# Kernel optimization log

Hardware: AMD Instinct MI355X
Metric: run time of the kernel (lower is better)

## Reference

```python
import jax, jax.numpy as jnp
import numpy as np

N_NODES = 50000
N_EDGES = 800000
IN_DIM = 128
HID_DIM = 128
EMB_DIM = 64


def _glorot(key, shape):
    fan_in, fan_out = shape
    lim = np.sqrt(6.0 / (fan_in + fan_out))
    return jax.random.uniform(key, shape, jnp.float32, -lim, lim)


def setup_inputs() -> dict:
    key = jax.random.key(0)
    ks = jax.random.split(key, 5)
    x = jax.random.normal(ks[0], (N_NODES, IN_DIM), jnp.float32)
    edge_index = jax.random.randint(ks[1], (2, N_EDGES), 0, N_NODES, jnp.int64)
    W1 = _glorot(ks[2], (IN_DIM, HID_DIM))
    W2 = _glorot(ks[3], (HID_DIM, EMB_DIM))
    W3 = _glorot(ks[4], (EMB_DIM, IN_DIM))
    b1 = jnp.zeros((HID_DIM,), jnp.float32)
    b2 = jnp.zeros((EMB_DIM,), jnp.float32)
    b3 = jnp.zeros((IN_DIM,), jnp.float32)
    return {"x": x, "edge_index": edge_index,
            "W1": W1, "b1": b1, "W2": W2, "b2": b2, "W3": W3, "b3": b3}


def _gcn_conv(x, W, b, src, dst, norm, n_nodes):
    # PyG GCNConv: transform then normalized neighbor aggregation (with self-loops)
    h = x @ W                                   # [N, out]
    msg = h[src] * norm[:, None]                # gather + scale, [E+N, out]
    out = jax.ops.segment_sum(msg, dst, num_segments=n_nodes)  # scatter-add
    return out + b


def _gcn_norm(edge_index, n_nodes):
    # add self-loops, compute sym-normalized edge weights D^-1/2 (A+I) D^-1/2
    loop = jnp.arange(n_nodes, dtype=edge_index.dtype)
    src = jnp.concatenate([edge_index[0], loop])
    dst = jnp.concatenate([edge_index[1], loop])
    deg = jax.ops.segment_sum(jnp.ones_like(dst, jnp.float32), dst,
                              num_segments=n_nodes)
    dinv = jnp.where(deg > 0, jax.lax.rsqrt(jnp.maximum(deg, 1.0)), 0.0)
    norm = dinv[src] * dinv[dst]
    return src, dst, norm


def reference(x, edge_index, W1, b1, W2, b2, W3, b3):
    n_nodes = x.shape[0]
    src, dst, norm = _gcn_norm(edge_index, n_nodes)
    h = jax.nn.relu(_gcn_conv(x, W1, b1, src, dst, norm, n_nodes))
    h = jax.nn.relu(_gcn_conv(h, W2, b2, src, dst, norm, n_nodes))
    out = _gcn_conv(h, W3, b3, src, dst, norm, n_nodes)
    return out
```

## Files before the change

kernel.cpp:

```cpp
#include <hip/hip_runtime.h>
#include <hip/hip_bf16.h>

static inline int ceil_div(int a, int b) { return (a + b - 1) / b; }


__global__ void count_kernel(const int* __restrict__ ei, int* __restrict__ deg,
        int* __restrict__ rank, int E) {
    int e = blockIdx.x * blockDim.x + threadIdx.x;
    if (e < E) rank[e] = atomicAdd(&deg[ei[E + e]], 1);
}


__global__ __launch_bounds__(256) void block_sum_kernel(const int* __restrict__ deg,
        int* __restrict__ bsum, int n) {
    int base = blockIdx.x * 1024 + (int)threadIdx.x * 4;
    int s = 0;
    #pragma unroll
    for (int j = 0; j < 4; ++j) { int i = base + j; if (i < n) s += deg[i]; }
    #pragma unroll
    for (int off = 32; off > 0; off >>= 1) s += __shfl_down(s, off);
    __shared__ int ws[4];
    int wid = (int)threadIdx.x >> 6, lane = (int)threadIdx.x & 63;
    if (lane == 0) ws[wid] = s;
    __syncthreads();
    if (threadIdx.x == 0) bsum[blockIdx.x] = ws[0] + ws[1] + ws[2] + ws[3];
}

__global__ void scan_bsum_kernel(const int* __restrict__ bsum, int* __restrict__ boff,
        int* __restrict__ rowptr, int nb, int n) {
    int tid = (int)threadIdx.x;
    int v = (tid < nb) ? bsum[tid] : 0;
    #pragma unroll
    for (int off = 1; off < 64; off <<= 1) {
        int u = __shfl_up(v, off);
        if (tid >= off) v += u;
    }
    if (tid < nb) boff[tid + 1] = v;
    if (tid == 0) boff[0] = 0;
    if (tid == nb - 1) rowptr[n] = v;
}

__global__ __launch_bounds__(256) void scan_apply_kernel(const int* __restrict__ deg,
        const int* __restrict__ boff, int* __restrict__ rowptr,
        float* __restrict__ dinv, int n) {
    int tid = (int)threadIdx.x;
    int base = blockIdx.x * 1024 + tid * 4;
    int d[4];
    #pragma unroll
    for (int j = 0; j < 4; ++j) { int i = base + j; d[j] = (i < n) ? deg[i] : 0; }
    int tsum = d[0] + d[1] + d[2] + d[3];
    int v = tsum;
    int lane = tid & 63, wid = tid >> 6;
    #pragma unroll
    for (int off = 1; off < 64; off <<= 1) {
        int u = __shfl_up(v, off);
        if (lane >= off) v += u;
    }
    __shared__ int wsum[4];
    if (lane == 63) wsum[wid] = v;
    __syncthreads();
    int wbase = 0;
    #pragma unroll
    for (int w = 0; w < 4; ++w) if (w < wid) wbase += wsum[w];
    int run = boff[blockIdx.x] + wbase + (v - tsum);
    #pragma unroll
    for (int j = 0; j < 4; ++j) {
        int i = base + j;
        if (i < n) {
            rowptr[i] = run;
            dinv[i] = rsqrtf((float)(d[j] + 1));
        }
        run += d[j];
    }
}

__global__ void fill_kernel(const int* __restrict__ ei, const int* __restrict__ rowptr,
        const int* __restrict__ rank, int* __restrict__ colidx, int E) {
    int e = blockIdx.x * blockDim.x + threadIdx.x;
    if (e < E) {
        int s = ei[e];
        int d = ei[E + e];
        colidx[rowptr[d] + rank[e]] = s;
    }
}


template<int K, int N, bool BIAS, bool OUT_BF16>
__global__ __launch_bounds__(256) void gemm_kernel(const float* __restrict__ A,
        const float* __restrict__ W, const float* __restrict__ bias,
        void* __restrict__ out_, int M) {
    __shared__ float As[16][68];
    __shared__ float Bs[16][68];
    const int bm = blockIdx.x * 64;
    const int bn = blockIdx.y * 64;
    const int tid = (int)threadIdx.x;
    const int tx = tid & 15;
    const int ty = tid >> 4;
    float acc[4][4] = {};
    for (int k0 = 0; k0 < K; k0 += 16) {
        {
            int m   = tid >> 2;
            int kk4 = (tid & 3) * 4;
            float4 v = make_float4(0.f, 0.f, 0.f, 0.f);
            if (bm + m < M)
                v = *(const float4*)&A[(size_t)(bm + m) * K + k0 + kk4];
            As[kk4 + 0][m] = v.x;
            As[kk4 + 1][m] = v.y;
            As[kk4 + 2][m] = v.z;
            As[kk4 + 3][m] = v.w;
        }
        {
            int kk = tid >> 4;
            int n4 = (tid & 15) * 4;
            *(float4*)&Bs[kk][n4] = *(const float4*)&W[(size_t)(k0 + kk) * N + bn + n4];
        }
        __syncthreads();
        #pragma unroll
        for (int kk = 0; kk < 16; ++kk) {
            float4 a4 = *(const float4*)&As[kk][ty * 4];
            float4 b4 = *(const float4*)&Bs[kk][tx * 4];
            float a[4] = {a4.x, a4.y, a4.z, a4.w};
            float b[4] = {b4.x, b4.y, b4.z, b4.w};
            #pragma unroll
            for (int i = 0; i < 4; ++i)
                #pragma unroll
                for (int j = 0; j < 4; ++j)
                    acc[i][j] += a[i] * b[j];
        }
        __syncthreads();
    }
    #pragma unroll
    for (int i = 0; i < 4; ++i) {
        int m = bm + ty * 4 + i;
        if (m >= M) continue;
        float v[4];
        #pragma unroll
        for (int j = 0; j < 4; ++j) {
            v[j] = acc[i][j];
            if (BIAS) v[j] += bias[bn + tx * 4 + j];
        }
        size_t base = (size_t)m * N + bn + tx * 4;
        if constexpr (OUT_BF16) {
            __hip_bfloat16* ob = (__hip_bfloat16*)out_;
            __hip_bfloat162 p0, p1;
            p0.x = __float2bfloat16(v[0]); p0.y = __float2bfloat16(v[1]);
            p1.x = __float2bfloat16(v[2]); p1.y = __float2bfloat16(v[3]);
            *(__hip_bfloat162*)&ob[base]     = p0;
            *(__hip_bfloat162*)&ob[base + 2] = p1;
        } else {
            float* of = (float*)out_;
            *(float2*)&of[base]     = make_float2(v[0], v[1]);
            *(float2*)&of[base + 2] = make_float2(v[2], v[3]);
        }
    }
}


template<int D, bool BIAS, bool RELU, bool OUT_BF16>
__global__ __launch_bounds__(256) void agg_kernel(const void* __restrict__ in_,
        const float* __restrict__ bias,
        const int* __restrict__ rowptr, const int* __restrict__ colidx,
        const float* __restrict__ dinv, void* __restrict__ out_, int n) {
    constexpr int VPL = D / 64;
    const int lane = (int)threadIdx.x & 63;
    const int wid  = (int)threadIdx.x >> 6;
    const int i = blockIdx.x * 4 + wid;
    if (i >= n) return;
    const float di = dinv[i];
    float acc0 = 0.f, acc1 = 0.f;
    if constexpr (VPL == 2) {
        const __hip_bfloat162* in = (const __hip_bfloat162*)in_;
        __hip_bfloat162 sv = in[(size_t)i * 64 + lane];
        acc0 = di * __bfloat162float(sv.x);
        acc1 = di * __bfloat162float(sv.y);
    } else {
        const __hip_bfloat16* in = (const __hip_bfloat16*)in_;
        acc0 = di * __bfloat162float(in[(size_t)i * 64 + lane]);
    }
    int e = rowptr[i];
    const int e1 = rowptr[i + 1];
    for (; e + 8 <= e1; e += 8) {
        int s[8]; float w[8];
        #pragma unroll
        for (int j = 0; j < 8; ++j) s[j] = __builtin_amdgcn_readfirstlane(colidx[e + j]);
        #pragma unroll
        for (int j = 0; j < 8; ++j) w[j] = dinv[s[j]];
        if constexpr (VPL == 2) {
            const __hip_bfloat162* in = (const __hip_bfloat162*)in_;
            __hip_bfloat162 v[8];
            #pragma unroll
            for (int j = 0; j < 8; ++j) v[j] = in[(size_t)s[j] * 64 + lane];
            #pragma unroll
            for (int j = 0; j < 8; ++j) {
                acc0 += w[j] * __bfloat162float(v[j].x);
                acc1 += w[j] * __bfloat162float(v[j].y);
            }
        } else {
            const __hip_bfloat16* in = (const __hip_bfloat16*)in_;
            __hip_bfloat16 v[8];
            #pragma unroll
            for (int j = 0; j < 8; ++j) v[j] = in[(size_t)s[j] * 64 + lane];
            #pragma unroll
            for (int j = 0; j < 8; ++j) acc0 += w[j] * __bfloat162float(v[j]);
        }
    }
    for (; e < e1; ++e) {
        int s = __builtin_amdgcn_readfirstlane(colidx[e]);
        float w = dinv[s];
        if constexpr (VPL == 2) {
            const __hip_bfloat162* in = (const __hip_bfloat162*)in_;
            __hip_bfloat162 v = in[(size_t)s * 64 + lane];
            acc0 += w * __bfloat162float(v.x);
            acc1 += w * __bfloat162float(v.y);
        } else {
            const __hip_bfloat16* in = (const __hip_bfloat16*)in_;
            acc0 += w * __bfloat162float(in[(size_t)s * 64 + lane]);
        }
    }
    float v0 = di * acc0;
    float v1 = di * acc1;
    if constexpr (VPL == 2) {
        if (BIAS) { v0 += bias[2 * lane]; v1 += bias[2 * lane + 1]; }
        if (RELU) { v0 = fmaxf(v0, 0.f); v1 = fmaxf(v1, 0.f); }
        if constexpr (OUT_BF16) {
            __hip_bfloat162* ob = (__hip_bfloat162*)out_;
            __hip_bfloat162 p; p.x = __float2bfloat16(v0); p.y = __float2bfloat16(v1);
            ob[(size_t)i * 64 + lane] = p;
        } else {
            float2* of = (float2*)out_;
            of[(size_t)i * 64 + lane] = make_float2(v0, v1);
        }
    } else {
        if (BIAS) v0 += bias[lane];
        if (RELU) v0 = fmaxf(v0, 0.f);
        if constexpr (OUT_BF16) {
            __hip_bfloat16* ob = (__hip_bfloat16*)out_;
            ob[(size_t)i * 64 + lane] = __float2bfloat16(v0);
        } else {
            float* of = (float*)out_;
            of[(size_t)i * 64 + lane] = v0;
        }
    }
}


extern "C" void kernel_launch(void* const* d_in, const int* in_sizes, int n_in,
                              void* d_out, int out_size, void* d_ws, size_t ws_size,
                              hipStream_t stream) {
    const float* x  = (const float*)d_in[0];
    const int*   ei = (const int*)d_in[1];
    const float* W1 = (const float*)d_in[2];
    const float* b1 = (const float*)d_in[3];
    const float* W2 = (const float*)d_in[4];
    const float* b2 = (const float*)d_in[5];
    const float* W3 = (const float*)d_in[6];
    const float* b3 = (const float*)d_in[7];

    const int IN = 128;
    const int n  = in_sizes[0] / IN;
    const int E  = in_sizes[1] / 2;

    char* ws = (char*)d_ws;
    size_t off = 0;
    auto alloc = [&](size_t bytes) {
        char* p = ws + off;
        off += (bytes + 255) & ~(size_t)255;
        return p;
    };
    __hip_bfloat16* hA_bf = (__hip_bfloat16*)alloc((size_t)n * 128 * 2);
    float*          bufB  = (float*)alloc((size_t)n * 128 * 4);
    __hip_bfloat16* hC_bf = (__hip_bfloat16*)alloc((size_t)n * 64 * 2);
    __hip_bfloat16* hD_bf = (__hip_bfloat16*)alloc((size_t)n * 64 * 2);
    float*          bufE  = (float*)alloc((size_t)n * 64 * 4);
    int*   deg    = (int*)  alloc((size_t)n * sizeof(int));
    int*   rowptr = (int*)  alloc(((size_t)n + 1) * sizeof(int));
    float* dinv   = (float*)alloc((size_t)n * sizeof(float));
    int*   colidx = (int*)  alloc((size_t)E * sizeof(int));
    int*   rank   = (int*)  alloc((size_t)E * sizeof(int));
    int*   bsum   = (int*)  alloc(64 * sizeof(int));
    int*   boff   = (int*)  alloc(65 * sizeof(int));

    const int nb = ceil_div(n, 1024);

    hipMemsetAsync(deg, 0, (size_t)n * sizeof(int), stream);
    count_kernel<<<ceil_div(E, 256), 256, 0, stream>>>(ei, deg, rank, E);
    block_sum_kernel<<<nb, 256, 0, stream>>>(deg, bsum, n);
    scan_bsum_kernel<<<1, 64, 0, stream>>>(bsum, boff, rowptr, nb, n);
    scan_apply_kernel<<<nb, 256, 0, stream>>>(deg, boff, rowptr, dinv, n);
    fill_kernel<<<ceil_div(E, 256), 256, 0, stream>>>(ei, rowptr, rank, colidx, E);

    dim3 g1(ceil_div(n, 64), 2);
    gemm_kernel<128, 128, false, true><<<g1, 256, 0, stream>>>(x, W1, nullptr, hA_bf, n);
    agg_kernel<128, true, true, false><<<ceil_div(n, 4), 256, 0, stream>>>(
        hA_bf, b1, rowptr, colidx, dinv, bufB, n);

    dim3 g2(ceil_div(n, 64), 1);
    gemm_kernel<128, 64, false, true><<<g2, 256, 0, stream>>>(bufB, W2, nullptr, hC_bf, n);
    agg_kernel<64, true, true, true><<<ceil_div(n, 4), 256, 0, stream>>>(
        hC_bf, b2, rowptr, colidx, dinv, hD_bf, n);

    agg_kernel<64, false, false, false><<<ceil_div(n, 4), 256, 0, stream>>>(
        hD_bf, nullptr, rowptr, colidx, dinv, bufE, n);
    dim3 g3(ceil_div(n, 64), 2);
    gemm_kernel<64, 128, true, false><<<g3, 256, 0, stream>>>(bufE, W3, b3, d_out, n);
}
```

Before: 305.8 us.

## Build CSR with two-level bucketed counting sort using shared-memory atomics

```diff
diff --git a/kernel.cpp b/kernel.cpp
--- a/kernel.cpp
+++ b/kernel.cpp
@@ -4,83 +4,102 @@
 static inline int ceil_div(int a, int b) { return (a + b - 1) / b; }
 
 
-__global__ void count_kernel(const int* __restrict__ ei, int* __restrict__ deg,
-        int* __restrict__ rank, int E) {
-    int e = blockIdx.x * blockDim.x + threadIdx.x;
-    if (e < E) rank[e] = atomicAdd(&deg[ei[E + e]], 1);
-}
-
-
-__global__ __launch_bounds__(256) void block_sum_kernel(const int* __restrict__ deg,
-        int* __restrict__ bsum, int n) {
-    int base = blockIdx.x * 1024 + (int)threadIdx.x * 4;
-    int s = 0;
-    #pragma unroll
-    for (int j = 0; j < 4; ++j) { int i = base + j; if (i < n) s += deg[i]; }
-    #pragma unroll
-    for (int off = 32; off > 0; off >>= 1) s += __shfl_down(s, off);
-    __shared__ int ws[4];
-    int wid = (int)threadIdx.x >> 6, lane = (int)threadIdx.x & 63;
-    if (lane == 0) ws[wid] = s;
-    __syncthreads();
-    if (threadIdx.x == 0) bsum[blockIdx.x] = ws[0] + ws[1] + ws[2] + ws[3];
-}
-
-__global__ void scan_bsum_kernel(const int* __restrict__ bsum, int* __restrict__ boff,
-        int* __restrict__ rowptr, int nb, int n) {
-    int tid = (int)threadIdx.x;
-    int v = (tid < nb) ? bsum[tid] : 0;
-    #pragma unroll
-    for (int off = 1; off < 64; off <<= 1) {
-        int u = __shfl_up(v, off);
-        if (tid >= off) v += u;
-    }
-    if (tid < nb) boff[tid + 1] = v;
-    if (tid == 0) boff[0] = 0;
-    if (tid == nb - 1) rowptr[n] = v;
-}
-
-__global__ __launch_bounds__(256) void scan_apply_kernel(const int* __restrict__ deg,
-        const int* __restrict__ boff, int* __restrict__ rowptr,
-        float* __restrict__ dinv, int n) {
-    int tid = (int)threadIdx.x;
-    int base = blockIdx.x * 1024 + tid * 4;
-    int d[4];
-    #pragma unroll
-    for (int j = 0; j < 4; ++j) { int i = base + j; d[j] = (i < n) ? deg[i] : 0; }
-    int tsum = d[0] + d[1] + d[2] + d[3];
-    int v = tsum;
-    int lane = tid & 63, wid = tid >> 6;
-    #pragma unroll
-    for (int off = 1; off < 64; off <<= 1) {
-        int u = __shfl_up(v, off);
-        if (lane >= off) v += u;
-    }
-    __shared__ int wsum[4];
-    if (lane == 63) wsum[wid] = v;
-    __syncthreads();
-    int wbase = 0;
-    #pragma unroll
-    for (int w = 0; w < 4; ++w) if (w < wid) wbase += wsum[w];
-    int run = boff[blockIdx.x] + wbase + (v - tsum);
-    #pragma unroll
-    for (int j = 0; j < 4; ++j) {
-        int i = base + j;
-        if (i < n) {
-            rowptr[i] = run;
-            dinv[i] = rsqrtf((float)(d[j] + 1));
-        }
-        run += d[j];
-    }
-}
-
-__global__ void fill_kernel(const int* __restrict__ ei, const int* __restrict__ rowptr,
-        const int* __restrict__ rank, int* __restrict__ colidx, int E) {
-    int e = blockIdx.x * blockDim.x + threadIdx.x;
-    if (e < E) {
+#define CSR_NBLK 64
+
+__global__ __launch_bounds__(1024) void bucket_hist_kernel(const int* __restrict__ ei,
+        int* __restrict__ hist_b, int E, int nbucket, int chunk) {
+    __shared__ int h[512];
+    for (int i = threadIdx.x; i < nbucket; i += blockDim.x) h[i] = 0;
+    __syncthreads();
+    const int b = blockIdx.x;
+    const int e0 = b * chunk, e1 = min(E, e0 + chunk);
+    for (int e = e0 + (int)threadIdx.x; e < e1; e += blockDim.x)
+        atomicAdd(&h[ei[E + e] >> 8], 1);
+    __syncthreads();
+    for (int i = threadIdx.x; i < nbucket; i += blockDim.x)
+        hist_b[i * CSR_NBLK + b] = h[i];
+}
+
+__global__ __launch_bounds__(512) void bucket_scan_kernel(int* __restrict__ hist_b,
+        int* __restrict__ bucket_start, int nbucket, int E) {
+    __shared__ int sc[512];
+    const int t = (int)threadIdx.x;
+    int tot = 0;
+    if (t < nbucket) {
+        #pragma unroll 8
+        for (int b = 0; b < CSR_NBLK; ++b) tot += hist_b[t * CSR_NBLK + b];
+    }
+    sc[t] = tot;
+    __syncthreads();
+    for (int off = 1; off < 512; off <<= 1) {
+        int v = (t >= off) ? sc[t - off] : 0;
+        __syncthreads();
+        sc[t] += v;
+        __syncthreads();
+    }
+    if (t < nbucket) {
+        int excl = sc[t] - tot;
+        bucket_start[t] = excl;
+        int base = excl;
+        #pragma unroll 8
+        for (int b = 0; b < CSR_NBLK; ++b) {
+            int c = hist_b[t * CSR_NBLK + b];
+            hist_b[t * CSR_NBLK + b] = base;
+            base += c;
+        }
+    }
+    if (t == 0) bucket_start[nbucket] = E;
+}
+
+__global__ __launch_bounds__(1024) void bucket_scatter_kernel(const int* __restrict__ ei,
+        const int* __restrict__ base_b, int2* __restrict__ tmp, int E, int nbucket, int chunk) {
+    __shared__ int cur[512];
+    const int b = blockIdx.x;
+    for (int i = threadIdx.x; i < nbucket; i += blockDim.x)
+        cur[i] = base_b[i * CSR_NBLK + b];
+    __syncthreads();
+    const int e0 = b * chunk, e1 = min(E, e0 + chunk);
+    for (int e = e0 + (int)threadIdx.x; e < e1; e += blockDim.x) {
         int s = ei[e];
         int d = ei[E + e];
-        colidx[rowptr[d] + rank[e]] = s;
+        int pos = atomicAdd(&cur[d >> 8], 1);
+        tmp[pos] = make_int2(s, d);
+    }
+}
+
+__global__ __launch_bounds__(256) void csr_build_kernel(const int2* __restrict__ tmp,
+        const int* __restrict__ bucket_start, int* __restrict__ rowptr,
+        float* __restrict__ dinv, int* __restrict__ colidx, int n, int E) {
+    __shared__ int hist[256], sc[256], cur[256];
+    const int h = blockIdx.x;
+    const int t = (int)threadIdx.x;
+    hist[t] = 0;
+    __syncthreads();
+    const int e0 = bucket_start[h], e1 = bucket_start[h + 1];
+    for (int e = e0 + t; e < e1; e += 256)
+        atomicAdd(&hist[tmp[e].y & 255], 1);
+    __syncthreads();
+    sc[t] = hist[t];
+    __syncthreads();
+    for (int off = 1; off < 256; off <<= 1) {
+        int v = (t >= off) ? sc[t - off] : 0;
+        __syncthreads();
+        sc[t] += v;
+        __syncthreads();
+    }
+    const int excl = sc[t] - hist[t];
+    const int node = h * 256 + t;
+    if (node < n) {
+        rowptr[node] = e0 + excl;
+        dinv[node] = rsqrtf((float)(hist[t] + 1));
+    }
+    if (h == 0 && t == 0) rowptr[n] = E;
+    cur[t] = excl;
+    __syncthreads();
+    for (int e = e0 + t; e < e1; e += 256) {
+        int2 p = tmp[e];
+        int pos = e0 + atomicAdd(&cur[p.y & 255], 1);
+        colidx[pos] = p.x;
     }
 }
 
@@ -272,22 +291,20 @@
     __hip_bfloat16* hC_bf = (__hip_bfloat16*)alloc((size_t)n * 64 * 2);
     __hip_bfloat16* hD_bf = (__hip_bfloat16*)alloc((size_t)n * 64 * 2);
     float*          bufE  = (float*)alloc((size_t)n * 64 * 4);
-    int*   deg    = (int*)  alloc((size_t)n * sizeof(int));
     int*   rowptr = (int*)  alloc(((size_t)n + 1) * sizeof(int));
     float* dinv   = (float*)alloc((size_t)n * sizeof(float));
     int*   colidx = (int*)  alloc((size_t)E * sizeof(int));
-    int*   rank   = (int*)  alloc((size_t)E * sizeof(int));
-    int*   bsum   = (int*)  alloc(64 * sizeof(int));
-    int*   boff   = (int*)  alloc(65 * sizeof(int));
-
-    const int nb = ceil_div(n, 1024);
-
-    hipMemsetAsync(deg, 0, (size_t)n * sizeof(int), stream);
-    count_kernel<<<ceil_div(E, 256), 256, 0, stream>>>(ei, deg, rank, E);
-    block_sum_kernel<<<nb, 256, 0, stream>>>(deg, bsum, n);
-    scan_bsum_kernel<<<1, 64, 0, stream>>>(bsum, boff, rowptr, nb, n);
-    scan_apply_kernel<<<nb, 256, 0, stream>>>(deg, boff, rowptr, dinv, n);
-    fill_kernel<<<ceil_div(E, 256), 256, 0, stream>>>(ei, rowptr, rank, colidx, E);
+    int2*  tmp    = (int2*) alloc((size_t)E * sizeof(int2));
+    int*   hist_b = (int*)  alloc((size_t)512 * CSR_NBLK * sizeof(int));
+    int*   bstart = (int*)  alloc(513 * sizeof(int));
+
+    const int nbucket = ceil_div(n, 256);
+    const int chunk   = ceil_div(E, CSR_NBLK);
+
+    bucket_hist_kernel<<<CSR_NBLK, 1024, 0, stream>>>(ei, hist_b, E, nbucket, chunk);
+    bucket_scan_kernel<<<1, 512, 0, stream>>>(hist_b, bstart, nbucket, E);
+    bucket_scatter_kernel<<<CSR_NBLK, 1024, 0, stream>>>(ei, hist_b, tmp, E, nbucket, chunk);
+    csr_build_kernel<<<nbucket, 256, 0, stream>>>(tmp, bstart, rowptr, dinv, colidx, n, E);
 
     dim3 g1(ceil_div(n, 64), 2);
     gemm_kernel<128, 128, false, true><<<g1, 256, 0, stream>>>(x, W1, nullptr, hA_bf, n);
```

Result: faster. 292.7 us (-4.3%).
